# Kernel tuning notes

Hardware: AMD Instinct MI355X
Metric: run time of the kernel (lower is better)

## Reference

```python
import jax, jax.numpy as jnp
import numpy as np


def setup_inputs() -> dict:
    key = jax.random.key(0)
    ks = jax.random.split(key, 12)
    N, T, V, C, O, IC, S = 32, 256, 25, 64, 64, 16, 3
    rn = lambda k, sh, s=1.0: jax.random.normal(k, sh, dtype=jnp.float32) * s
    return {
        "x": rn(ks[0], (N, T, V, C)),
        "A": jax.random.uniform(ks[1], (S, V, V), dtype=jnp.float32),
        "PA": rn(ks[2], (S, V, V), 0.01),
        "weight_A": jax.random.uniform(ks[3], (4,), dtype=jnp.float32),
        "Wa": rn(ks[4], (S, C, IC), 1.0 / np.sqrt(C)),
        "ba": rn(ks[5], (S, IC), 0.01),
        "Wb": rn(ks[6], (S, C, IC), 1.0 / np.sqrt(C)),
        "bb": rn(ks[7], (S, IC), 0.01),
        "Wd": rn(ks[8], (S, C, O), 1.0 / np.sqrt(C)),
        "bd": rn(ks[9], (S, O), 0.01),
        "gamma": jax.random.uniform(ks[10], (O,), dtype=jnp.float32),
        "beta": rn(ks[11], (O,), 0.1),
    }


def reference(x, A, PA, weight_A, Wa, ba, Wb, bb, Wd, bd, gamma, beta):
    # unit_gcn_confirm forward (in_channels == out_channels, so `down` = identity)
    N, T, V, C = x.shape
    S, _, IC = Wa.shape
    BN_EPS = 1e-5

    # A = w0 * A_static + w1 * softmax(PA)  -> (S, V, V)
    A_comb = weight_A[0] * A + weight_A[1] * jax.nn.softmax(PA, axis=-1)

    # per-subset Q/K projections: (S, N, T, V, IC)
    qa = jnp.einsum('ntvc,sci->sntvi', x, Wa) + ba[:, None, None, None, :]
    kb = jnp.einsum('ntvc,sci->sntvi', x, Wb) + bb[:, None, None, None, :]

    # A1: time-flattened attention over nodes, scale sqrt(IC*T) -> (S, N, V, V)
    A1 = jax.nn.softmax(
        jnp.einsum('sntui,sntvi->snuv', qa, kb) / jnp.sqrt(jnp.float32(IC * T)),
        axis=-1)
    # A2: per-frame attention over nodes, scale sqrt(IC) -> (S, N, T, V, V)
    A2 = jax.nn.softmax(
        jnp.einsum('sntui,sntvi->sntuv', qa, kb) / jnp.sqrt(jnp.float32(IC)),
        axis=-1)

    # combined adjacency per subset: (S, N, T, V, V)
    A_in = (A_comb[:, None, None, :, :]
            + weight_A[2] * A1[:, :, None, :, :]
            + weight_A[3] * A2)

    # message passing + per-subset output linear, summed over subsets
    z = jnp.einsum('sntuv,ntvc->sntuc', A_in, x)             # (S, N, T, V, C)
    y = jnp.einsum('sntuc,sco->ntuo', z, Wd) + bd.sum(0)     # (N, T, V, O)

    # BatchNorm2d in inference mode (running_mean=0, running_var=1)
    y = y * (gamma / jnp.sqrt(1.0 + BN_EPS)) + beta

    # residual (down = identity since in_channels == out_channels) + relu
    return jax.nn.relu(y + x)
```

## Files before the change

kernel.cpp:

```cpp
#include <hip/hip_runtime.h>
#include <hip/hip_bf16.h>

typedef __hip_bfloat16 bf16;
typedef __attribute__((ext_vector_type(8))) short short8;
typedef __attribute__((ext_vector_type(4))) float f32x4;

#define S  3
#define V  25
#define C  64
#define O  64
#define IC 16
#define NN 32
#define TT 256
#define TB 2
#define TCH 8

__device__ __forceinline__ float b2f(bf16 v) { return __bfloat162float(v); }

__device__ __forceinline__ float ldv(const void* p, size_t i, int f32) {
    return f32 ? ((const float*)p)[i] : b2f(((const bf16*)p)[i]);
}

__device__ __forceinline__ unsigned short f2bf(float f) {
    bf16 h = __float2bfloat16(f);
    return *(unsigned short*)&h;
}

__global__ __launch_bounds__(256) void k_prep(
    const void* __restrict__ x,
    const void* __restrict__ A, const void* __restrict__ PA,
    const void* __restrict__ wA,
    const void* __restrict__ Wa, const void* __restrict__ Wb,
    const void* __restrict__ Wd,
    float* __restrict__ A_comb, float* __restrict__ S1,
    unsigned short* __restrict__ wprep, int* __restrict__ flagp) {
    __shared__ int sflag;
    if (threadIdx.x < 64) {
        const bf16* p = (const bf16*)x;
        int bad = 0;
        #pragma unroll
        for (int k = 0; k < 32; k++) {
            float v = b2f(p[threadIdx.x + k * 64]);
            bad |= !(v > -1000.f && v < 1000.f);
        }
        unsigned long long m = __ballot(bad);
        if (threadIdx.x == 0) {
            sflag = (m != 0ull) ? 1 : 0;
            if (blockIdx.x == 0) *flagp = sflag;
        }
    }
    __syncthreads();
    int f32 = sflag;

    int g = blockIdx.x * 256 + threadIdx.x;
    int stride = gridDim.x * 256;

    for (int w = g; w < 60000; w += stride) S1[w] = 0.f;

    for (int w = g; w < 3456; w += stride) {
        int s = w / 1152, r = w % 1152, i = r / 72, c = r % 72;
        unsigned short va = 0, vb = 0;
        if (c < 64) {
            va = f2bf(ldv(Wa, (size_t)s * 1024 + c * 16 + i, f32));
            vb = f2bf(ldv(Wb, (size_t)s * 1024 + c * 16 + i, f32));
        }
        wprep[s * 6912 + i * 72 + c] = va;
        wprep[s * 6912 + 1152 + i * 72 + c] = vb;
    }
    for (int w = g; w < 13824; w += stride) {
        int s = w / 4608, r = w % 4608, o = r / 72, c = r % 72;
        unsigned short vd = 0;
        if (c < 64) vd = f2bf(ldv(Wd, (size_t)s * 4096 + c * 64 + o, f32));
        wprep[s * 6912 + 2304 + o * 72 + c] = vd;
    }

    if (g < S * V) {
        float w0 = ldv(wA, 0, f32), w1 = ldv(wA, 1, f32);
        float vals[V];
        float m = -1e30f;
        for (int v = 0; v < V; v++) { vals[v] = ldv(PA, g * V + v, f32); m = fmaxf(m, vals[v]); }
        float sum = 0.f;
        for (int v = 0; v < V; v++) { vals[v] = __expf(vals[v] - m); sum += vals[v]; }
        float inv = 1.f / sum;
        for (int v = 0; v < V; v++)
            A_comb[g * V + v] = w0 * ldv(A, g * V + v, f32) + w1 * vals[v] * inv;
    }
}

#define P1_QK(sidx, QB, KB) do {                                              \
    const unsigned short* wat_ = wprep + (size_t)(sidx) * 6912;               \
    const unsigned short* wbt_ = wat_ + 1152;                                 \
    short8 wa0 = *(const short8*)&wat_[lm * 72 + kq * 8];                     \
    short8 wa1 = *(const short8*)&wat_[lm * 72 + 32 + kq * 8];                \
    short8 wb0 = *(const short8*)&wbt_[lm * 72 + kq * 8];                     \
    short8 wb1 = *(const short8*)&wbt_[lm * 72 + 32 + kq * 8];                \
    f32x4 q = __builtin_amdgcn_mfma_f32_16x16x32_bf16(xa0, wa0, (f32x4){0.f,0.f,0.f,0.f}, 0, 0, 0); \
    q = __builtin_amdgcn_mfma_f32_16x16x32_bf16(xa1, wa1, q, 0, 0, 0);        \
    f32x4 k = __builtin_amdgcn_mfma_f32_16x16x32_bf16(xa0, wb0, (f32x4){0.f,0.f,0.f,0.f}, 0, 0, 0); \
    k = __builtin_amdgcn_mfma_f32_16x16x32_bf16(xa1, wb1, k, 0, 0, 0);        \
    _Pragma("unroll")                                                         \
    for (int reg = 0; reg < 4; reg++) {                                       \
        (QB)[(drow0 + reg) * 20 + lm] = f2bf(q[reg] + rbq[sidx]);             \
        (KB)[(drow0 + reg) * 20 + lm] = f2bf(k[reg] + rbk[sidx]);             \
    }                                                                         \
} while (0)

#define E_ACC(AC, QB, KB) do {                                                \
    short8 a_ = *(const short8*)&(QB)[(tsel + ur0 + lm) * 20 + ksel];         \
    short8 b_ = *(const short8*)&(KB)[(tsel + vc0 + lm) * 20 + ksel];         \
    (AC) = __builtin_amdgcn_mfma_f32_16x16x32_bf16(a_, b_, (AC), 0, 0, 0);    \
} while (0)

#define STAGE_XB(TTOFF) do {                                                  \
    if (f32) {                                                                \
        const float4* xp = (const float4*)x + (size_t)(n * TT + t0 + (TTOFF)) * 400; \
        for (int w = tid; w < 800; w += 256) {                                \
            int t = w / 400, r = w % 400, u = r >> 4, c4 = r & 15;            \
            float4 v = xp[w];                                                 \
            unsigned short h[4] = {f2bf(v.x), f2bf(v.y), f2bf(v.z), f2bf(v.w)}; \
            *(uint2*)&xb[(t * 32 + u) * 72 + c4 * 4] = *(uint2*)h;            \
        }                                                                     \
    } else {                                                                  \
        const unsigned int* xp = (const unsigned int*)x;                      \
        size_t base2 = (size_t)(n * TT + t0 + (TTOFF)) * V * C / 2;           \
        for (int w = tid; w < 1600; w += 256) {                               \
            int t = w / 800, r = w % 800, u = r >> 5, c2 = r & 31;            \
            ((unsigned int*)xb)[(t * 32 + u) * 36 + c2] = xp[base2 + (size_t)(t * V + u) * 32 + c2]; \
        }                                                                     \
    }                                                                         \
} while (0)

__global__ __launch_bounds__(256) void k_s1(
    const void* __restrict__ x,
    const unsigned short* __restrict__ wprep,
    const void* __restrict__ ba, const void* __restrict__ bb,
    float* __restrict__ S1g, const int* __restrict__ flagp) {
    int f32 = *flagp;
    int tchunk = blockIdx.x, n = blockIdx.y;
    int tid = threadIdx.x;
    int lane = tid & 63, wv = tid >> 6;
    int lm = lane & 15, kq = lane >> 4;

    __shared__ __align__(16) unsigned short xb[64 * 72];
    __shared__ __align__(16) unsigned short qb[3][64 * 20];
    __shared__ __align__(16) unsigned short kb_[3][64 * 20];

    float rbq[3], rbk[3];
    #pragma unroll
    for (int s = 0; s < 3; s++) {
        rbq[s] = ldv(ba, s * IC + lm, f32);
        rbk[s] = ldv(bb, s * IC + lm, f32);
    }

    int mrow = wv * 16 + lm;
    int drow0 = wv * 16 + (kq << 2);
    int ur0 = ((wv >> 1) & 1) << 4;
    int vc0 = (wv & 1) << 4;
    int t0 = tchunk * TCH;
    int tsel = (kq >> 1) << 5;
    int ksel = (kq & 1) << 3;

    f32x4 acc0 = {0.f,0.f,0.f,0.f}, acc1 = {0.f,0.f,0.f,0.f}, acc2 = {0.f,0.f,0.f,0.f};

    STAGE_XB(0);
    __syncthreads();

    for (int pp = 0; pp < TCH / 2; pp++) {
        short8 xa0 = *(const short8*)&xb[mrow * 72 + kq * 8];
        short8 xa1 = *(const short8*)&xb[mrow * 72 + 32 + kq * 8];
        P1_QK(0, qb[0], kb_[0]);
        P1_QK(1, qb[1], kb_[1]);
        P1_QK(2, qb[2], kb_[2]);
        __syncthreads();
        E_ACC(acc0, qb[0], kb_[0]);
        E_ACC(acc1, qb[1], kb_[1]);
        E_ACC(acc2, qb[2], kb_[2]);
        if (pp < TCH / 2 - 1) STAGE_XB(2 * pp + 2);
        __syncthreads();
    }

    {
        int u = ur0 + (kq << 2), v = vc0 + lm;
        float* d0 = S1g + (size_t)n * 625;
        float* d1 = S1g + ((size_t)NN + n) * 625;
        float* d2 = S1g + ((size_t)2 * NN + n) * 625;
        #pragma unroll
        for (int reg = 0; reg < 4; reg++) {
            if (u + reg < V && v < V) {
                atomicAdd(&d0[(u + reg) * 25 + v], acc0[reg]);
                atomicAdd(&d1[(u + reg) * 25 + v], acc1[reg]);
                atomicAdd(&d2[(u + reg) * 25 + v], acc2[reg]);
            }
        }
    }
}

__global__ void k_a1(float* __restrict__ S1g, const float* __restrict__ A_comb,
                     const void* __restrict__ wA, const int* __restrict__ flagp) {
    int f32 = *flagp;
    float w2 = ldv(wA, 2, f32);
    int sn = blockIdx.x;
    int s = sn / NN;
    int u = threadIdx.x;
    if (u >= V) return;
    float* row = S1g + (size_t)sn * V * V + u * V;
    const float* ac = A_comb + (size_t)(s * V + u) * V;
    const float scale = 1.0f / 64.0f;
    float vals[V];
    float m = -1e30f;
    for (int v = 0; v < V; v++) { vals[v] = row[v] * scale; m = fmaxf(m, vals[v]); }
    float sum = 0.f;
    for (int v = 0; v < V; v++) { vals[v] = __expf(vals[v] - m); sum += vals[v]; }
    float inv = w2 / sum;
    for (int v = 0; v < V; v++) row[v] = ac[v] + vals[v] * inv;
}

__global__ __launch_bounds__(256, 5) void k_main(
    const void* __restrict__ x,
    const void* __restrict__ ba, const void* __restrict__ bb,
    const void* __restrict__ bd,
    const void* __restrict__ gamma, const void* __restrict__ beta,
    const void* __restrict__ wA,
    const unsigned short* __restrict__ wprep,
    const float* __restrict__ ac1g,
    void* __restrict__ outp, const int* __restrict__ flagp) {
    int f32 = *flagp;
    int bx = blockIdx.x;
    int n = bx >> 7, tc = bx & 127;
    int t0 = tc * TB;
    int tid = threadIdx.x;
    int lane = tid & 63, wv = tid >> 6;
    int lm = lane & 15, kq = lane >> 4;

    __shared__ __align__(16) unsigned short xb[64 * 72];
    __shared__ __align__(16) unsigned short qab[64 * 40];
    __shared__ __align__(16) unsigned short kbb[64 * 40];
    __shared__ __align__(16) unsigned short xwtb[2 * 64 * 40];
    __shared__ float gs[O], bts[O], bds[O];

    if (f32) {
        const float4* xp = (const float4*)x + (size_t)(n * TT + t0) * 400;
        for (int w = tid; w < 800; w += 256) {
            int t = w / 400, r = w % 400, u = r >> 4, c4 = r & 15;
            float4 v = xp[w];
            unsigned short h[4] = {f2bf(v.x), f2bf(v.y), f2bf(v.z), f2bf(v.w)};
            *(uint2*)&xb[(t * 32 + u) * 72 + c4 * 4] = *(uint2*)h;
        }
    } else {
        const unsigned int* xp = (const unsigned int*)x;
        size_t base2 = (size_t)(n * TT + t0) * V * C / 2;
        for (int w = tid; w < 1600; w += 256) {
            int t = w / 800, r = w % 800, u = r >> 5, c2 = r & 31;
            ((unsigned int*)xb)[(t * 32 + u) * 36 + c2] = xp[base2 + (size_t)(t * V + u) * 32 + c2];
        }
    }
    for (int w = tid; w < 14 * 36; w += 256) {
        int idx = w / 36, word = w % 36;
        int row = (idx < 7) ? (25 + idx) : (32 + 25 + idx - 7);
        ((unsigned int*)xb)[row * 36 + word] = 0;
    }
    for (int w = tid; w < 512; w += 256) {
        int r = w >> 3, cw = 8 + (w & 7);
        ((unsigned int*)qab)[r * 20 + cw] = 0;
        ((unsigned int*)kbb)[r * 20 + cw] = 0;
    }
    if (tid < O) {
        bds[tid] = ldv(bd, tid, f32) + ldv(bd, O + tid, f32) + ldv(bd, 2 * O + tid, f32);
        gs[tid] = ldv(gamma, tid, f32) * rsqrtf(1.f + 1e-5f);
        bts[tid] = ldv(beta, tid, f32);
    }
    float w3 = ldv(wA, 3, f32);

    f32x4 acc[4];
    #pragma unroll
    for (int nt = 0; nt < 4; nt++) acc[nt] = (f32x4){0.f, 0.f, 0.f, 0.f};

    int t_ = wv >> 1;
    int mrow = wv * 16 + lm;
    int drow0 = wv * 16 + (kq << 2);
    int ub = ((wv & 1) << 4) + (kq << 2);

    __syncthreads();

    short8 xa0 = *(const short8*)&xb[mrow * 72 + kq * 8];
    short8 xa1 = *(const short8*)&xb[mrow * 72 + 32 + kq * 8];

    for (int s = 0; s < S; s++) {
        const unsigned short* watg = wprep + s * 6912;
        const unsigned short* wbtg = watg + 1152;
        const unsigned short* wdtg = watg + 2304;
        const float* acn = ac1g + ((size_t)s * NN + n) * 625;

        {
            short8 wa0 = *(const short8*)&watg[lm * 72 + kq * 8];
            short8 wa1 = *(const short8*)&watg[lm * 72 + 32 + kq * 8];
            short8 wb0 = *(const short8*)&wbtg[lm * 72 + kq * 8];
            short8 wb1 = *(const short8*)&wbtg[lm * 72 + 32 + kq * 8];
            float bq_c = ldv(ba, s * IC + lm, f32);
            float bk_c = ldv(bb, s * IC + lm, f32);
            f32x4 q = __builtin_amdgcn_mfma_f32_16x16x32_bf16(xa0, wa0, (f32x4){0.f,0.f,0.f,0.f}, 0, 0, 0);
            q = __builtin_amdgcn_mfma_f32_16x16x32_bf16(xa1, wa1, q, 0, 0, 0);
            f32x4 k = __builtin_amdgcn_mfma_f32_16x16x32_bf16(xa0, wb0, (f32x4){0.f,0.f,0.f,0.f}, 0, 0, 0);
            k = __builtin_amdgcn_mfma_f32_16x16x32_bf16(xa1, wb1, k, 0, 0, 0);
            #pragma unroll
            for (int reg = 0; reg < 4; reg++) {
                qab[(drow0 + reg) * 40 + lm] = f2bf(q[reg] + bq_c);
                kbb[(drow0 + reg) * 40 + lm] = f2bf(k[reg] + bk_c);
            }
        }
        {
            #pragma unroll
            for (int nt = 0; nt < 4; nt++) {
                short8 wd0 = *(const short8*)&wdtg[(nt * 16 + lm) * 72 + kq * 8];
                short8 wd1 = *(const short8*)&wdtg[(nt * 16 + lm) * 72 + 32 + kq * 8];
                f32x4 xw = __builtin_amdgcn_mfma_f32_16x16x32_bf16(xa0, wd0, (f32x4){0.f,0.f,0.f,0.f}, 0, 0, 0);
                xw = __builtin_amdgcn_mfma_f32_16x16x32_bf16(xa1, wd1, xw, 0, 0, 0);
                unsigned short h[4] = {f2bf(xw[0]), f2bf(xw[1]), f2bf(xw[2]), f2bf(xw[3])};
                *(uint2*)&xwtb[t_ * 2560 + (nt * 16 + lm) * 40 + ub] = *(uint2*)h;
            }
        }
        __syncthreads();

        {
            short8 aq = *(const short8*)&qab[mrow * 40 + kq * 8];
            short8 bk0 = *(const short8*)&kbb[(t_ * 32 + lm) * 40 + kq * 8];
            short8 bk1 = *(const short8*)&kbb[(t_ * 32 + 16 + lm) * 40 + kq * 8];
            f32x4 e0 = __builtin_amdgcn_mfma_f32_16x16x32_bf16(aq, bk0, (f32x4){0.f,0.f,0.f,0.f}, 0, 0, 0);
            f32x4 e1 = __builtin_amdgcn_mfma_f32_16x16x32_bf16(aq, bk1, (f32x4){0.f,0.f,0.f,0.f}, 0, 0, 0);
            #pragma unroll
            for (int reg = 0; reg < 4; reg++) {
                float p0 = __expf(e0[reg] * 0.25f);
                float p1 = (lm < V - 16) ? __expf(e1[reg] * 0.25f) : 0.f;
                float pr = p0 + p1;
                pr += __shfl_xor(pr, 1);
                pr += __shfl_xor(pr, 2);
                pr += __shfl_xor(pr, 4);
                pr += __shfl_xor(pr, 8);
                float si = w3 / pr;
                int u = ub + reg;
                int uc = (u < V) ? u : 0;
                float a0v = (u < V) ? (acn[uc * 25 + lm] + si * p0) : 0.f;
                float a1v = (u < V && lm < V - 16) ? (acn[uc * 25 + 16 + lm] + si * p1) : 0.f;
                qab[(drow0 + reg) * 40 + lm] = f2bf(a0v);
                qab[(drow0 + reg) * 40 + 16 + lm] = f2bf(a1v);
            }
        }
        {
            short8 aA = *(const short8*)&qab[mrow * 40 + kq * 8];
            #pragma unroll
            for (int nt = 0; nt < 4; nt++) {
                short8 bx8 = *(const short8*)&xwtb[t_ * 2560 + (nt * 16 + lm) * 40 + kq * 8];
                acc[nt] = __builtin_amdgcn_mfma_f32_16x16x32_bf16(aA, bx8, acc[nt], 0, 0, 0);
            }
            if (s < S - 1) {
                #pragma unroll
                for (int reg = 0; reg < 4; reg++)
                    qab[(drow0 + reg) * 40 + 16 + lm] = 0;
            }
        }
        __syncthreads();
    }

    if (f32) {
        #pragma unroll
        for (int nt = 0; nt < 4; nt++) {
            int o = nt * 16 + lm;
            float g = gs[o], bt_ = bts[o], bsum = bds[o];
            #pragma unroll
            for (int reg = 0; reg < 4; reg++) {
                int grow = drow0 + reg;
                int t = grow >> 5, u = grow & 31;
                if (u < V) {
                    float xres = b2f(*(const bf16*)&xb[grow * 72 + o]);
                    float yv = fmaxf((acc[nt][reg] + bsum) * g + bt_ + xres, 0.f);
                    size_t ob = (size_t)((n * TT + t0 + t) * V + u) * O + o;
                    ((float*)outp)[ob] = yv;
                }
            }
        }
    } else {
        unsigned short* ep = xwtb;
        #pragma unroll
        for (int nt = 0; nt < 4; nt++) {
            int o = nt * 16 + lm;
            float g = gs[o], bt_ = bts[o], bsum = bds[o];
            #pragma unroll
            for (int reg = 0; reg < 4; reg++) {
                int grow = drow0 + reg;
                int t = grow >> 5, u = grow & 31;
                if (u < V) {
                    float xres = b2f(*(const bf16*)&xb[grow * 72 + o]);
                    float yv = fmaxf((acc[nt][reg] + bsum) * g + bt_ + xres, 0.f);
                    ep[(t * V + u) * O + o] = f2bf(yv);
                }
            }
        }
        __syncthreads();
        uint4* outv = (uint4*)((bf16*)outp + (size_t)(n * TT + t0) * V * O);
        const uint4* epv = (const uint4*)ep;
        for (int w = tid; w < 400; w += 256) outv[w] = epv[w];
    }
}

extern "C" void kernel_launch(void* const* d_in, const int* in_sizes, int n_in,
                              void* d_out, int out_size, void* d_ws, size_t ws_size,
                              hipStream_t stream) {
    const void* x     = d_in[0];
    const void* A     = d_in[1];
    const void* PA    = d_in[2];
    const void* wA    = d_in[3];
    const void* Wa    = d_in[4];
    const void* ba    = d_in[5];
    const void* Wb    = d_in[6];
    const void* bb    = d_in[7];
    const void* Wd    = d_in[8];
    const void* bd    = d_in[9];
    const void* gamma = d_in[10];
    const void* beta  = d_in[11];

    int*   flagp  = (int*)d_ws;
    float* wsf    = (float*)d_ws;
    float* A_comb = wsf + 64;
    float* S1     = wsf + 2048;
    unsigned short* wprep = (unsigned short*)(wsf + 65536);

    k_prep<<<256, 256, 0, stream>>>(x, A, PA, wA, Wa, Wb, Wd, A_comb, S1, wprep, flagp);
    k_s1<<<dim3(TT / TCH, NN), 256, 0, stream>>>(x, wprep, ba, bb, S1, flagp);
    k_a1<<<S * NN, 64, 0, stream>>>(S1, A_comb, wA, flagp);
    k_main<<<NN * TT / TB, 256, 0, stream>>>(x, ba, bb, bd, gamma, beta, wA,
                                             wprep, S1, d_out, flagp);
}
```

Baseline: 212.5 us.

## Give each wave a whole frame to drop per-subset block barriers

Each block now handles four frames instead of two, and each wave owns one full frame (32 rows, two 16-row halves). That lets the Q/K, attention softmax and message-passing MFMAs run inside the wave without the two __syncthreads per subset. The x·Wd product goes into a small per-wave LDS scratch and is consumed right away instead of through a block-shared buffer. Adjacency values are prefetched into registers, and the BN/bias params are read straight from global instead of shared memory. This costs more registers and LDS per block, so occupancy drops (launch bounds 5→3) and there are half as many blocks.

```diff
diff --git a/kernel.cpp b/kernel.cpp
--- a/kernel.cpp
+++ b/kernel.cpp
@@ -12,7 +12,7 @@
 #define IC 16
 #define NN 32
 #define TT 256
-#define TB 2
+#define TB 4
 #define TCH 8
 
 __device__ __forceinline__ float b2f(bf16 v) { return __bfloat162float(v); }
@@ -215,7 +215,26 @@
     for (int v = 0; v < V; v++) row[v] = ac[v] + vals[v] * inv;
 }
 
-__global__ __launch_bounds__(256, 5) void k_main(
+#define SM_HALF(EA, EB, UH) do {                                              \
+    _Pragma("unroll")                                                         \
+    for (int reg = 0; reg < 4; reg++) {                                       \
+        float p0 = __expf((EA)[reg] * 0.25f);                                 \
+        float p1 = (lm < V - 16) ? __expf((EB)[reg] * 0.25f) : 0.f;           \
+        float pr = p0 + p1;                                                   \
+        pr += __shfl_xor(pr, 1);                                              \
+        pr += __shfl_xor(pr, 2);                                              \
+        pr += __shfl_xor(pr, 4);                                              \
+        pr += __shfl_xor(pr, 8);                                              \
+        float si = w3 / pr;                                                   \
+        int u = (UH) * 16 + (kq << 2) + reg;                                  \
+        float a0v = (u < V) ? (pa0[UH][reg] + si * p0) : 0.f;                 \
+        float a1v = (u < V && lm < V - 16) ? (pa1[UH][reg] + si * p1) : 0.f;  \
+        qab[(wv * 32 + (UH) * 16 + (kq << 2) + reg) * 40 + lm] = f2bf(a0v);   \
+        qab[(wv * 32 + (UH) * 16 + (kq << 2) + reg) * 40 + 16 + lm] = f2bf(a1v); \
+    }                                                                         \
+} while (0)
+
+__global__ __launch_bounds__(256, 3) void k_main(
     const void* __restrict__ x,
     const void* __restrict__ ba, const void* __restrict__ bb,
     const void* __restrict__ bd,
@@ -226,21 +245,21 @@
     void* __restrict__ outp, const int* __restrict__ flagp) {
     int f32 = *flagp;
     int bx = blockIdx.x;
-    int n = bx >> 7, tc = bx & 127;
+    int n = bx >> 6, tc = bx & 63;
     int t0 = tc * TB;
     int tid = threadIdx.x;
     int lane = tid & 63, wv = tid >> 6;
     int lm = lane & 15, kq = lane >> 4;
 
-    __shared__ __align__(16) unsigned short xb[64 * 72];
-    __shared__ __align__(16) unsigned short qab[64 * 40];
-    __shared__ __align__(16) unsigned short kbb[64 * 40];
-    __shared__ __align__(16) unsigned short xwtb[2 * 64 * 40];
-    __shared__ float gs[O], bts[O], bds[O];
+    __shared__ __align__(16) unsigned short pool[22016];
+    unsigned short* xb  = pool;
+    unsigned short* qab = pool + 9216;
+    unsigned short* kbb = pool + 14336;
+    unsigned short* xws = pool + 19456 + wv * 640;
 
     if (f32) {
         const float4* xp = (const float4*)x + (size_t)(n * TT + t0) * 400;
-        for (int w = tid; w < 800; w += 256) {
+        for (int w = tid; w < 1600; w += 256) {
             int t = w / 400, r = w % 400, u = r >> 4, c4 = r & 15;
             float4 v = xp[w];
             unsigned short h[4] = {f2bf(v.x), f2bf(v.y), f2bf(v.z), f2bf(v.w)};
@@ -249,156 +268,169 @@
     } else {
         const unsigned int* xp = (const unsigned int*)x;
         size_t base2 = (size_t)(n * TT + t0) * V * C / 2;
-        for (int w = tid; w < 1600; w += 256) {
+        for (int w = tid; w < 3200; w += 256) {
             int t = w / 800, r = w % 800, u = r >> 5, c2 = r & 31;
             ((unsigned int*)xb)[(t * 32 + u) * 36 + c2] = xp[base2 + (size_t)(t * V + u) * 32 + c2];
         }
     }
-    for (int w = tid; w < 14 * 36; w += 256) {
+    for (int w = tid; w < 28 * 36; w += 256) {
         int idx = w / 36, word = w % 36;
-        int row = (idx < 7) ? (25 + idx) : (32 + 25 + idx - 7);
-        ((unsigned int*)xb)[row * 36 + word] = 0;
-    }
-    for (int w = tid; w < 512; w += 256) {
+        int t = idx / 7, ur = 25 + idx % 7;
+        ((unsigned int*)xb)[(t * 32 + ur) * 36 + word] = 0;
+    }
+    for (int w = tid; w < 1024; w += 256) {
         int r = w >> 3, cw = 8 + (w & 7);
         ((unsigned int*)qab)[r * 20 + cw] = 0;
         ((unsigned int*)kbb)[r * 20 + cw] = 0;
     }
-    if (tid < O) {
-        bds[tid] = ldv(bd, tid, f32) + ldv(bd, O + tid, f32) + ldv(bd, 2 * O + tid, f32);
-        gs[tid] = ldv(gamma, tid, f32) * rsqrtf(1.f + 1e-5f);
-        bts[tid] = ldv(beta, tid, f32);
-    }
     float w3 = ldv(wA, 3, f32);
 
-    f32x4 acc[4];
+    f32x4 acc0[4], acc1[4];
     #pragma unroll
-    for (int nt = 0; nt < 4; nt++) acc[nt] = (f32x4){0.f, 0.f, 0.f, 0.f};
-
-    int t_ = wv >> 1;
-    int mrow = wv * 16 + lm;
-    int drow0 = wv * 16 + (kq << 2);
-    int ub = ((wv & 1) << 4) + (kq << 2);
+    for (int nt = 0; nt < 4; nt++) {
+        acc0[nt] = (f32x4){0.f, 0.f, 0.f, 0.f};
+        acc1[nt] = (f32x4){0.f, 0.f, 0.f, 0.f};
+    }
 
     __syncthreads();
 
-    short8 xa0 = *(const short8*)&xb[mrow * 72 + kq * 8];
-    short8 xa1 = *(const short8*)&xb[mrow * 72 + 32 + kq * 8];
+    short8 xa00 = *(const short8*)&xb[(wv * 32 + lm) * 72 + kq * 8];
+    short8 xa01 = *(const short8*)&xb[(wv * 32 + lm) * 72 + 32 + kq * 8];
+    short8 xa10 = *(const short8*)&xb[(wv * 32 + 16 + lm) * 72 + kq * 8];
+    short8 xa11 = *(const short8*)&xb[(wv * 32 + 16 + lm) * 72 + 32 + kq * 8];
 
     for (int s = 0; s < S; s++) {
         const unsigned short* watg = wprep + s * 6912;
         const unsigned short* wbtg = watg + 1152;
         const unsigned short* wdtg = watg + 2304;
         const float* acn = ac1g + ((size_t)s * NN + n) * 625;
+        float bq_c = ldv(ba, s * IC + lm, f32);
+        float bk_c = ldv(bb, s * IC + lm, f32);
 
         {
             short8 wa0 = *(const short8*)&watg[lm * 72 + kq * 8];
             short8 wa1 = *(const short8*)&watg[lm * 72 + 32 + kq * 8];
             short8 wb0 = *(const short8*)&wbtg[lm * 72 + kq * 8];
             short8 wb1 = *(const short8*)&wbtg[lm * 72 + 32 + kq * 8];
-            float bq_c = ldv(ba, s * IC + lm, f32);
-            float bk_c = ldv(bb, s * IC + lm, f32);
-            f32x4 q = __builtin_amdgcn_mfma_f32_16x16x32_bf16(xa0, wa0, (f32x4){0.f,0.f,0.f,0.f}, 0, 0, 0);
-            q = __builtin_amdgcn_mfma_f32_16x16x32_bf16(xa1, wa1, q, 0, 0, 0);
-            f32x4 k = __builtin_amdgcn_mfma_f32_16x16x32_bf16(xa0, wb0, (f32x4){0.f,0.f,0.f,0.f}, 0, 0, 0);
-            k = __builtin_amdgcn_mfma_f32_16x16x32_bf16(xa1, wb1, k, 0, 0, 0);
+            f32x4 q0 = __builtin_amdgcn_mfma_f32_16x16x32_bf16(xa00, wa0, (f32x4){0.f,0.f,0.f,0.f}, 0, 0, 0);
+            q0 = __builtin_amdgcn_mfma_f32_16x16x32_bf16(xa01, wa1, q0, 0, 0, 0);
+            f32x4 q1 = __builtin_amdgcn_mfma_f32_16x16x32_bf16(xa10, wa0, (f32x4){0.f,0.f,0.f,0.f}, 0, 0, 0);
+            q1 = __builtin_amdgcn_mfma_f32_16x16x32_bf16(xa11, wa1, q1, 0, 0, 0);
+            f32x4 k0 = __builtin_amdgcn_mfma_f32_16x16x32_bf16(xa00, wb0, (f32x4){0.f,0.f,0.f,0.f}, 0, 0, 0);
+            k0 = __builtin_amdgcn_mfma_f32_16x16x32_bf16(xa01, wb1, k0, 0, 0, 0);
+            f32x4 k1 = __builtin_amdgcn_mfma_f32_16x16x32_bf16(xa10, wb0, (f32x4){0.f,0.f,0.f,0.f}, 0, 0, 0);
+            k1 = __builtin_amdgcn_mfma_f32_16x16x32_bf16(xa11, wb1, k1, 0, 0, 0);
+            int r0 = wv * 32 + (kq << 2);
             #pragma unroll
             for (int reg = 0; reg < 4; reg++) {
-                qab[(drow0 + reg) * 40 + lm] = f2bf(q[reg] + bq_c);
-                kbb[(drow0 + reg) * 40 + lm] = f2bf(k[reg] + bk_c);
+                qab[(r0 + reg) * 40 + lm]      = f2bf(q0[reg] + bq_c);
+                qab[(r0 + 16 + reg) * 40 + lm] = f2bf(q1[reg] + bq_c);
+                kbb[(r0 + reg) * 40 + lm]      = f2bf(k0[reg] + bk_c);
+                kbb[(r0 + 16 + reg) * 40 + lm] = f2bf(k1[reg] + bk_c);
             }
         }
+
+        float pa0[2][4], pa1[2][4];
+        #pragma unroll
+        for (int uh = 0; uh < 2; uh++)
+            #pragma unroll
+            for (int reg = 0; reg < 4; reg++) {
+                int u = uh * 16 + (kq << 2) + reg;
+                int uc = (u < V) ? u : 0;
+                pa0[uh][reg] = acn[uc * 25 + lm];
+                pa1[uh][reg] = (lm < V - 16) ? acn[uc * 25 + 16 + lm] : 0.f;
+            }
+
         {
+            short8 aq0 = *(const short8*)&qab[(wv * 32 + lm) * 40 + kq * 8];
+            short8 aq1 = *(const short8*)&qab[(wv * 32 + 16 + lm) * 40 + kq * 8];
+            short8 bk0 = *(const short8*)&kbb[(wv * 32 + lm) * 40 + kq * 8];
+            short8 bk1 = *(const short8*)&kbb[(wv * 32 + 16 + lm) * 40 + kq * 8];
+            f32x4 e00 = __builtin_amdgcn_mfma_f32_16x16x32_bf16(aq0, bk0, (f32x4){0.f,0.f,0.f,0.f}, 0, 0, 0);
+            f32x4 e01 = __builtin_amdgcn_mfma_f32_16x16x32_bf16(aq0, bk1, (f32x4){0.f,0.f,0.f,0.f}, 0, 0, 0);
+            f32x4 e10 = __builtin_amdgcn_mfma_f32_16x16x32_bf16(aq1, bk0, (f32x4){0.f,0.f,0.f,0.f}, 0, 0, 0);
+            f32x4 e11 = __builtin_amdgcn_mfma_f32_16x16x32_bf16(aq1, bk1, (f32x4){0.f,0.f,0.f,0.f}, 0, 0, 0);
+            SM_HALF(e00, e01, 0);
+            SM_HALF(e10, e11, 1);
+        }
+
+        {
+            short8 aA0 = *(const short8*)&qab[(wv * 32 + lm) * 40 + kq * 8];
+            short8 aA1 = *(const short8*)&qab[(wv * 32 + 16 + lm) * 40 + kq * 8];
             #pragma unroll
             for (int nt = 0; nt < 4; nt++) {
                 short8 wd0 = *(const short8*)&wdtg[(nt * 16 + lm) * 72 + kq * 8];
                 short8 wd1 = *(const short8*)&wdtg[(nt * 16 + lm) * 72 + 32 + kq * 8];
-                f32x4 xw = __builtin_amdgcn_mfma_f32_16x16x32_bf16(xa0, wd0, (f32x4){0.f,0.f,0.f,0.f}, 0, 0, 0);
-                xw = __builtin_amdgcn_mfma_f32_16x16x32_bf16(xa1, wd1, xw, 0, 0, 0);
-                unsigned short h[4] = {f2bf(xw[0]), f2bf(xw[1]), f2bf(xw[2]), f2bf(xw[3])};
-                *(uint2*)&xwtb[t_ * 2560 + (nt * 16 + lm) * 40 + ub] = *(uint2*)h;
+                f32x4 xw0 = __builtin_amdgcn_mfma_f32_16x16x32_bf16(xa00, wd0, (f32x4){0.f,0.f,0.f,0.f}, 0, 0, 0);
+                xw0 = __builtin_amdgcn_mfma_f32_16x16x32_bf16(xa01, wd1, xw0, 0, 0, 0);
+                f32x4 xw1 = __builtin_amdgcn_mfma_f32_16x16x32_bf16(xa10, wd0, (f32x4){0.f,0.f,0.f,0.f}, 0, 0, 0);
+                xw1 = __builtin_amdgcn_mfma_f32_16x16x32_bf16(xa11, wd1, xw1, 0, 0, 0);
+                unsigned short h0[4] = {f2bf(xw0[0]), f2bf(xw0[1]), f2bf(xw0[2]), f2bf(xw0[3])};
+                unsigned short h1[4] = {f2bf(xw1[0]), f2bf(xw1[1]), f2bf(xw1[2]), f2bf(xw1[3])};
+                *(uint2*)&xws[lm * 40 + (kq << 2)]      = *(uint2*)h0;
+                *(uint2*)&xws[lm * 40 + 16 + (kq << 2)] = *(uint2*)h1;
+                short8 bx8 = *(const short8*)&xws[lm * 40 + kq * 8];
+                acc0[nt] = __builtin_amdgcn_mfma_f32_16x16x32_bf16(aA0, bx8, acc0[nt], 0, 0, 0);
+                acc1[nt] = __builtin_amdgcn_mfma_f32_16x16x32_bf16(aA1, bx8, acc1[nt], 0, 0, 0);
             }
         }
-        __syncthreads();
-
-        {
-            short8 aq = *(const short8*)&qab[mrow * 40 + kq * 8];
-            short8 bk0 = *(const short8*)&kbb[(t_ * 32 + lm) * 40 + kq * 8];
-            short8 bk1 = *(const short8*)&kbb[(t_ * 32 + 16 + lm) * 40 + kq * 8];
-            f32x4 e0 = __builtin_amdgcn_mfma_f32_16x16x32_bf16(aq, bk0, (f32x4){0.f,0.f,0.f,0.f}, 0, 0, 0);
-            f32x4 e1 = __builtin_amdgcn_mfma_f32_16x16x32_bf16(aq, bk1, (f32x4){0.f,0.f,0.f,0.f}, 0, 0, 0);
+        if (s < S - 1) {
             #pragma unroll
             for (int reg = 0; reg < 4; reg++) {
-                float p0 = __expf(e0[reg] * 0.25f);
-                float p1 = (lm < V - 16) ? __expf(e1[reg] * 0.25f) : 0.f;
-                float pr = p0 + p1;
-                pr += __shfl_xor(pr, 1);
-                pr += __shfl_xor(pr, 2);
-                pr += __shfl_xor(pr, 4);
-                pr += __shfl_xor(pr, 8);
-                float si = w3 / pr;
-                int u = ub + reg;
-                int uc = (u < V) ? u : 0;
-                float a0v = (u < V) ? (acn[uc * 25 + lm] + si * p0) : 0.f;
-                float a1v = (u < V && lm < V - 16) ? (acn[uc * 25 + 16 + lm] + si * p1) : 0.f;
-                qab[(drow0 + reg) * 40 + lm] = f2bf(a0v);
-                qab[(drow0 + reg) * 40 + 16 + lm] = f2bf(a1v);
+                qab[(wv * 32 + (kq << 2) + reg) * 40 + 16 + lm] = 0;
+                qab[(wv * 32 + 16 + (kq << 2) + reg) * 40 + 16 + lm] = 0;
             }
         }
-        {
-            short8 aA = *(const short8*)&qab[mrow * 40 + kq * 8];
-            #pragma unroll
-            for (int nt = 0; nt < 4; nt++) {
-                short8 bx8 = *(const short8*)&xwtb[t_ * 2560 + (nt * 16 + lm) * 40 + kq * 8];
-                acc[nt] = __builtin_amdgcn_mfma_f32_16x16x32_bf16(aA, bx8, acc[nt], 0, 0, 0);
-            }
-            if (s < S - 1) {
-                #pragma unroll
-                for (int reg = 0; reg < 4; reg++)
-                    qab[(drow0 + reg) * 40 + 16 + lm] = 0;
-            }
-        }
-        __syncthreads();
-    }
+    }
+
+    __syncthreads();
 
     if (f32) {
         #pragma unroll
         for (int nt = 0; nt < 4; nt++) {
             int o = nt * 16 + lm;
-            float g = gs[o], bt_ = bts[o], bsum = bds[o];
-            #pragma unroll
-            for (int reg = 0; reg < 4; reg++) {
-                int grow = drow0 + reg;
-                int t = grow >> 5, u = grow & 31;
-                if (u < V) {
-                    float xres = b2f(*(const bf16*)&xb[grow * 72 + o]);
-                    float yv = fmaxf((acc[nt][reg] + bsum) * g + bt_ + xres, 0.f);
-                    size_t ob = (size_t)((n * TT + t0 + t) * V + u) * O + o;
-                    ((float*)outp)[ob] = yv;
+            float g = ldv(gamma, o, 1) * rsqrtf(1.f + 1e-5f);
+            float bt_ = ldv(beta, o, 1);
+            float bsum = ldv(bd, o, 1) + ldv(bd, O + o, 1) + ldv(bd, 2 * O + o, 1);
+            #pragma unroll
+            for (int uh = 0; uh < 2; uh++)
+                #pragma unroll
+                for (int reg = 0; reg < 4; reg++) {
+                    int u = uh * 16 + (kq << 2) + reg;
+                    if (u < V) {
+                        float av = uh ? acc1[nt][reg] : acc0[nt][reg];
+                        float xres = b2f(*(const bf16*)&xb[(wv * 32 + u) * 72 + o]);
+                        float yv = fmaxf((av + bsum) * g + bt_ + xres, 0.f);
+                        size_t ob = (size_t)((n * TT + t0 + wv) * V + u) * O + o;
+                        ((float*)outp)[ob] = yv;
+                    }
                 }
-            }
         }
     } else {
-        unsigned short* ep = xwtb;
+        unsigned short* ep = pool + 9216;
         #pragma unroll
         for (int nt = 0; nt < 4; nt++) {
             int o = nt * 16 + lm;
-            float g = gs[o], bt_ = bts[o], bsum = bds[o];
-            #pragma unroll
-            for (int reg = 0; reg < 4; reg++) {
-                int grow = drow0 + reg;
-                int t = grow >> 5, u = grow & 31;
-                if (u < V) {
-                    float xres = b2f(*(const bf16*)&xb[grow * 72 + o]);
-                    float yv = fmaxf((acc[nt][reg] + bsum) * g + bt_ + xres, 0.f);
-                    ep[(t * V + u) * O + o] = f2bf(yv);
+            float g = ldv(gamma, o, 0) * rsqrtf(1.f + 1e-5f);
+            float bt_ = ldv(beta, o, 0);
+            float bsum = ldv(bd, o, 0) + ldv(bd, O + o, 0) + ldv(bd, 2 * O + o, 0);
+            #pragma unroll
+            for (int uh = 0; uh < 2; uh++)
+                #pragma unroll
+                for (int reg = 0; reg < 4; reg++) {
+                    int u = uh * 16 + (kq << 2) + reg;
+                    if (u < V) {
+                        float av = uh ? acc1[nt][reg] : acc0[nt][reg];
+                        float xres = b2f(*(const bf16*)&xb[(wv * 32 + u) * 72 + o]);
+                        float yv = fmaxf((av + bsum) * g + bt_ + xres, 0.f);
+                        ep[(wv * V + u) * O + o] = f2bf(yv);
+                    }
                 }
-            }
         }
         __syncthreads();
         uint4* outv = (uint4*)((bf16*)outp + (size_t)(n * TT + t0) * V * O);
         const uint4* epv = (const uint4*)ep;
-        for (int w = tid; w < 400; w += 256) outv[w] = epv[w];
+        for (int w = tid; w < 800; w += 256) outv[w] = epv[w];
     }
 }
 
```

New measurement: 190.7 us. 10.3% less time.
